# Kernel tuning notes

Hardware: AMD Instinct MI355X
Metric: run time of the kernel (lower is better)

## Reference

```python
import jax, jax.numpy as jnp
import numpy as np

B, T, C = 2, 2048, 768
H, N_LEFT = 12, 6
D = C // H


def setup_inputs() -> dict:
    key = jax.random.key(0)
    ks = jax.random.split(key, 4)
    x = jax.random.normal(ks[0], (B, T, C), dtype=jnp.float32)
    attention_mask = jnp.ones((B, T), dtype=jnp.int32)
    Wqkv_w = jax.random.normal(ks[1], (3 * C, C), dtype=jnp.float32) * (C ** -0.5)
    Wqkv_b = jnp.zeros((3 * C,), dtype=jnp.float32)
    Wo_w = jax.random.normal(ks[2], (C, C), dtype=jnp.float32) * (C ** -0.5)
    Wo_b = jnp.zeros((C,), dtype=jnp.float32)
    return {"x": x, "attention_mask": attention_mask, "Wqkv_w": Wqkv_w,
            "Wqkv_b": Wqkv_b, "Wo_w": Wo_w, "Wo_b": Wo_b}


def _attend(q, k, v, mask):
    # q,k,v: [B,h,T,D]; mask: [B,1,T,T] additive
    s = jnp.einsum('bhqd,bhkd->bhqk', q, k) * (D ** -0.5) + mask
    a = jax.nn.softmax(s.astype(jnp.float32), axis=-1).astype(q.dtype)
    return jnp.einsum('bhqk,bhkd->bhqd', a, v)


def reference(x, attention_mask, Wqkv_w, Wqkv_b, Wo_w, Wo_b):
    neg = jnp.finfo(x.dtype).min
    # padding mask [B,1,1,T]: 0 where valid, neg where padded
    pad = (1.0 - attention_mask.astype(x.dtype))[:, None, None, :] * neg
    i = jnp.arange(T)
    tri = (i[None, :] > i[:, None]).astype(x.dtype) * neg   # triu(neg, 1)
    left_mask = tri[None, None] + pad                        # causal (look left)
    right_mask = tri.T[None, None] + pad                     # anti-causal (look right)

    qkv = (x @ Wqkv_w.T + Wqkv_b).reshape(B, T, 3, H, D)
    qkv = jnp.transpose(qkv, (0, 3, 2, 1, 4))                # [B,H,3,T,D]
    q, k, v = qkv[:, :, 0], qkv[:, :, 1], qkv[:, :, 2]

    lc = _attend(q[:, :N_LEFT], k[:, :N_LEFT], v[:, :N_LEFT], left_mask)
    rc = _attend(q[:, N_LEFT:], k[:, N_LEFT:], v[:, N_LEFT:], right_mask)
    ctx = jnp.concatenate([lc, rc], axis=1)                  # [B,H,T,D]
    ctx = jnp.transpose(ctx, (0, 2, 1, 3)).reshape(B, T, C)
    out = ctx @ Wo_w.T + Wo_b
    return out
```

## Files before the change

### kernel.cpp

```cpp
#include <hip/hip_runtime.h>


typedef unsigned short u16;
typedef __bf16 bf16x8 __attribute__((ext_vector_type(8)));
typedef float fx4 __attribute__((ext_vector_type(4)));
typedef unsigned short u16x8 __attribute__((ext_vector_type(8)));
typedef unsigned short u16x4 __attribute__((ext_vector_type(4)));
typedef _Float16 hx4 __attribute__((ext_vector_type(4)));
typedef __fp16 fp16x2 __attribute__((ext_vector_type(2)));

#define T_SEQ 2048
#define C_DIM 768
#define NHEAD 12
#define HDIM  64
#define NITEMS 768
#define LOG2E_8 0.18033688f

__device__ __forceinline__ u16 f2bf(float f) {
  unsigned u = __float_as_uint(f);
  u += 0x7fffu + ((u >> 16) & 1u);
  return (u16)(u >> 16);
}
__device__ __forceinline__ u16 f2h(float f) {
  union { _Float16 h; u16 u; } cv; cv.h = (_Float16)f; return cv.u;
}

__device__ __forceinline__ void gl2lds16(const u16* g, u16* l) {
  __builtin_amdgcn_global_load_lds(
      (const __attribute__((address_space(1))) void*)g,
      (__attribute__((address_space(3))) void*)l, 16, 0, 0);
}

__global__ void cvt_swz_k(const float* __restrict__ x,
                          const float* __restrict__ wqkv,
                          const float* __restrict__ wo,
                          u16* __restrict__ out) {
  int i = blockIdx.x * blockDim.x + threadIdx.x;
  if (i >= 688128) return;
  int m = i / 96;
  int c8 = (i - m * 96) << 3;
  const float* src;
  if (m < 4096)       src = x    + (size_t)m * C_DIM + c8;
  else if (m < 6400)  src = wqkv + (size_t)(m - 4096) * C_DIM + c8;
  else                src = wo   + (size_t)(m - 6400) * C_DIM + c8;
  fx4 a = *(const fx4*)src, b = *(const fx4*)(src + 4);
  u16x8 o;
  #pragma unroll
  for (int j = 0; j < 4; ++j) { o[j] = f2bf(a[j]); o[4 + j] = f2bf(b[j]); }
  *(u16x8*)&out[(size_t)m * C_DIM + (c8 ^ ((m & 7) << 3))] = o;
}

__global__ void maskcvt_k(const int* __restrict__ am, float* __restrict__ mf,
                          unsigned* __restrict__ fbits, int* __restrict__ cnt) {
  int i = blockIdx.x * blockDim.x + threadIdx.x;
  if (i < 4096) mf[i] = am[i] ? 0.f : -1e30f;
  if (blockIdx.x == 16) {
    int t = threadIdx.x;
    if (t == 0) cnt[0] = 0;
    if (t < 64) {
      int bb = t >> 5, kt = t & 31;
      const int* seg = am + (bb << 11) + (kt << 6);
      int anyz = 0;
      for (int j = 0; j < 64; ++j) anyz |= (seg[j] == 0);
      unsigned long long bal = __ballot(anyz != 0);
      if (t == 0)  fbits[0] = (unsigned)(bal & 0xffffffffull);
      if (t == 32) fbits[1] = (unsigned)(bal >> 32);
    }
  }
}

__device__ __forceinline__ void gemm_core_64x128(const u16* __restrict__ A,
                                                 const u16* __restrict__ B,
                                                 int m0, int n0,
                                                 u16* As, u16* Bs,
                                                 fx4 acc[4][2]) {
  const int tid = threadIdx.x;
  const int lane = tid & 63, wv = tid >> 6;
  const int wn = wv << 5;
  const int lr = lane & 15, lg = lane >> 4;
  const int swk = (lr & 7) << 3;
  const int scol = (tid & 7) << 3;
  #pragma unroll
  for (int mt = 0; mt < 4; ++mt)
    #pragma unroll
    for (int nt = 0; nt < 2; ++nt) acc[mt][nt] = fx4{0.f, 0.f, 0.f, 0.f};

  #pragma unroll
  for (int p = 0; p < 2; ++p) {
    int row = (tid >> 3) + (p << 5);
    gl2lds16(&A[(size_t)(m0 + row) * C_DIM + scol], &As[(row << 6) + scol]);
  }
  #pragma unroll
  for (int p = 0; p < 4; ++p) {
    int row = (tid >> 3) + (p << 5);
    gl2lds16(&B[(size_t)(n0 + row) * C_DIM + scol], &Bs[(row << 6) + scol]);
  }

  int buf = 0;
  for (int k0 = 0; k0 < C_DIM; k0 += 64, buf ^= 1) {
    __syncthreads();
    if (k0 + 64 < C_DIM) {
      u16* Ad = &As[(buf ^ 1) << 12];
      u16* Bd = &Bs[(buf ^ 1) << 13];
      #pragma unroll
      for (int p = 0; p < 2; ++p) {
        int row = (tid >> 3) + (p << 5);
        gl2lds16(&A[(size_t)(m0 + row) * C_DIM + k0 + 64 + scol], &Ad[(row << 6) + scol]);
      }
      #pragma unroll
      for (int p = 0; p < 4; ++p) {
        int row = (tid >> 3) + (p << 5);
        gl2lds16(&B[(size_t)(n0 + row) * C_DIM + k0 + 64 + scol], &Bd[(row << 6) + scol]);
      }
    }
    const u16* Ab = &As[buf << 12];
    const u16* Bb = &Bs[buf << 13];
    #pragma unroll
    for (int kk = 0; kk < 64; kk += 32) {
      bf16x8 af[4], bfr[2];
      #pragma unroll
      for (int mt = 0; mt < 4; ++mt)
        af[mt] = *(const bf16x8*)&Ab[((mt * 16 + lr) << 6) + ((kk + lg * 8) ^ swk)];
      #pragma unroll
      for (int nt = 0; nt < 2; ++nt)
        bfr[nt] = *(const bf16x8*)&Bb[((wn + nt * 16 + lr) << 6) + ((kk + lg * 8) ^ swk)];
      #pragma unroll
      for (int mt = 0; mt < 4; ++mt)
        #pragma unroll
        for (int nt = 0; nt < 2; ++nt)
          acc[mt][nt] = __builtin_amdgcn_mfma_f32_16x16x32_bf16(
              af[mt], bfr[nt], acc[mt][nt], 0, 0, 0);
    }
  }
}

__global__ __launch_bounds__(256) void gemm_qkv_k(
    const u16* __restrict__ A, const u16* __restrict__ B,
    const float* __restrict__ bias,
    u16* __restrict__ qb, u16* __restrict__ kswz, u16* __restrict__ vswz) {
  __shared__ __align__(16) u16 As[2][64 * 64];
  __shared__ __align__(16) u16 Bs[2][128 * 64];
  int m0 = blockIdx.y << 6, n0 = blockIdx.x << 7;
  fx4 acc[4][2];
  gemm_core_64x128(A, B, m0, n0, &As[0][0], &Bs[0][0], acc);

  const int tid = threadIdx.x, lane = tid & 63, wv = tid >> 6;
  const int wn = wv << 5;
  const int lr = lane & 15, lg = lane >> 4;
  const int part = n0 / 768;
  const int n0r = n0 - part * 768;
  const int bb = m0 >> 11, kt = (m0 >> 6) & 31;
  u16* Sc = &Bs[0][0];
  __syncthreads();

  if (part < 2) {
    #pragma unroll
    for (int nt = 0; nt < 2; ++nt) {
      int nl = wn + nt * 16 + lr;
      float bv = bias[n0 + nl];
      #pragma unroll
      for (int mt = 0; mt < 4; ++mt) {
        #pragma unroll
        for (int r = 0; r < 4; ++r) {
          int m = mt * 16 + lg * 4 + r;
          Sc[(m << 7) + (nl ^ ((m & 15) << 2))] = f2bf(acc[mt][nt][r] + bv);
        }
      }
    }
    __syncthreads();
    int c4 = (tid & 31) << 2;
    int ng = n0r + c4;
    int h = ng >> 6, d = ng & 63;
    int bh = bb * NHEAD + h;
    #pragma unroll
    for (int p = 0; p < 8; ++p) {
      int m = (tid >> 5) + (p << 3);
      u16x4 v = *(const u16x4*)&Sc[(m << 7) + (c4 ^ ((m & 15) << 2))];
      if (part == 0) {
        int t = (m0 & 2047) + m;
        *(u16x4*)&qb[(((size_t)bh << 11) + t) * HDIM + d] = v;
      } else {
        *(u16x4*)&kswz[((size_t)(bh * 32 + kt) << 12) + (m << 6) +
                       (d ^ ((m & 7) << 3))] = v;
      }
    }
  } else {
    #pragma unroll
    for (int nt = 0; nt < 2; ++nt) {
      int nl = wn + nt * 16 + lr;
      float bv = bias[n0 + nl];
      #pragma unroll
      for (int mt = 0; mt < 4; ++mt) {
        u16x4 pk;
        #pragma unroll
        for (int r = 0; r < 4; ++r) pk[r] = f2h(acc[mt][nt][r] + bv);
        int m4 = (mt << 2) + lg;
        *(u16x4*)&Sc[(nl << 6) + ((m4 ^ (nl & 15)) << 2)] = pk;
      }
    }
    __syncthreads();
    int tr4 = tid & 15;
    #pragma unroll
    for (int p = 0; p < 8; ++p) {
      int nl = (tid >> 4) + (p << 4);
      int ng = n0r + nl;
      int h = ng >> 6, d = ng & 63;
      u16x4 v = *(const u16x4*)&Sc[(nl << 6) + ((tr4 ^ (nl & 15)) << 2)];
      size_t tile = (size_t)((bb * NHEAD + h) * 32 + kt) << 12;
      *(u16x4*)&vswz[tile + (d << 6) + ((tr4 ^ (d & 15)) << 2)] = v;
    }
  }
}

__device__ __forceinline__ void gemm_core_64x64(const u16* __restrict__ A,
                                                const u16* __restrict__ B,
                                                int m0, int n0,
                                                u16* As, u16* Bs,
                                                fx4 acc[2][2]) {
  const int tid = threadIdx.x;
  const int lane = tid & 63, wv = tid >> 6;
  const int wm = (wv & 1) << 5, wn = (wv >> 1) << 5;
  const int lr = lane & 15, lg = lane >> 4;
  const int swk = (lr & 7) << 3;
  const int scol = (tid & 7) << 3;
  #pragma unroll
  for (int mt = 0; mt < 2; ++mt)
    #pragma unroll
    for (int nt = 0; nt < 2; ++nt) acc[mt][nt] = fx4{0.f, 0.f, 0.f, 0.f};

  #pragma unroll
  for (int p = 0; p < 2; ++p) {
    int row = (tid >> 3) + (p << 5);
    gl2lds16(&A[(size_t)(m0 + row) * C_DIM + scol], &As[(row << 6) + scol]);
    gl2lds16(&B[(size_t)(n0 + row) * C_DIM + scol], &Bs[(row << 6) + scol]);
  }

  int buf = 0;
  for (int k0 = 0; k0 < C_DIM; k0 += 64, buf ^= 1) {
    __syncthreads();
    if (k0 + 64 < C_DIM) {
      u16* Ad = &As[(buf ^ 1) << 12];
      u16* Bd = &Bs[(buf ^ 1) << 12];
      #pragma unroll
      for (int p = 0; p < 2; ++p) {
        int row = (tid >> 3) + (p << 5);
        gl2lds16(&A[(size_t)(m0 + row) * C_DIM + k0 + 64 + scol], &Ad[(row << 6) + scol]);
        gl2lds16(&B[(size_t)(n0 + row) * C_DIM + k0 + 64 + scol], &Bd[(row << 6) + scol]);
      }
    }
    const u16* Ab = &As[buf << 12];
    const u16* Bb = &Bs[buf << 12];
    #pragma unroll
    for (int kk = 0; kk < 64; kk += 32) {
      bf16x8 af[2], bfr[2];
      #pragma unroll
      for (int mt = 0; mt < 2; ++mt)
        af[mt] = *(const bf16x8*)&Ab[((wm + mt * 16 + lr) << 6) + ((kk + lg * 8) ^ swk)];
      #pragma unroll
      for (int nt = 0; nt < 2; ++nt)
        bfr[nt] = *(const bf16x8*)&Bb[((wn + nt * 16 + lr) << 6) + ((kk + lg * 8) ^ swk)];
      #pragma unroll
      for (int mt = 0; mt < 2; ++mt)
        #pragma unroll
        for (int nt = 0; nt < 2; ++nt)
          acc[mt][nt] = __builtin_amdgcn_mfma_f32_16x16x32_bf16(
              af[mt], bfr[nt], acc[mt][nt], 0, 0, 0);
    }
  }
}

__global__ __launch_bounds__(256) void gemm_out_k(
    const u16* __restrict__ A, const u16* __restrict__ B,
    const float* __restrict__ bias, float* __restrict__ out) {
  __shared__ __align__(16) u16 As[2][64 * 64];
  __shared__ __align__(16) u16 Bs[2][64 * 64];
  int m0 = blockIdx.y << 6, n0 = blockIdx.x << 6;
  fx4 acc[2][2];
  gemm_core_64x64(A, B, m0, n0, &As[0][0], &Bs[0][0], acc);

  const int tid = threadIdx.x, lane = tid & 63, wv = tid >> 6;
  const int wm = (wv & 1) << 5, wn = (wv >> 1) << 5;
  const int lr = lane & 15, lg = lane >> 4;
  #pragma unroll
  for (int nt = 0; nt < 2; ++nt) {
    int n = n0 + wn + nt * 16 + lr;
    float bv = bias[n];
    #pragma unroll
    for (int mt = 0; mt < 2; ++mt) {
      #pragma unroll
      for (int r = 0; r < 4; ++r) {
        int m = m0 + wm + mt * 16 + lg * 4 + r;
        out[(size_t)m * C_DIM + n] = acc[mt][nt][r] + bv;
      }
    }
  }
}

__global__ __launch_bounds__(256) void attn_k(
    const u16* __restrict__ q, const u16* __restrict__ kswz,
    const u16* __restrict__ vswz, const float* __restrict__ maskf,
    const unsigned* __restrict__ fbits,
    u16* __restrict__ ctx, int* __restrict__ counter) {
  __shared__ __align__(16) u16 Ks[2][4096];
  __shared__ __align__(16) u16 Vt[2][4096];
  __shared__ int s_w;

  const int tid = threadIdx.x, lane = tid & 63, wv = tid >> 6;
  const int lr = lane & 15, lg = lane >> 4;
  const int swk = (lr & 7) << 3;
  const int swv = (lr & 15) << 2;

  for (;;) {
    if (tid == 0) s_w = atomicAdd(counter, 1);
    __syncthreads();
    int w = s_w;
    if (w >= NITEMS) break;
    int qslot = w / 24, bh = w - qslot * 24;
    int bb = bh / NHEAD, h = bh - bb * NHEAD;
    bool causal = (h < 6);
    int qt = causal ? (31 - qslot) : qslot;
    int kt0 = causal ? 0 : qt;
    int kt1 = causal ? qt : 31;
    size_t tile_base = (size_t)(bh * 32) << 12;
    unsigned fb = fbits[bb];

    {
      const u16* kg = kswz + tile_base + ((size_t)kt0 << 12);
      const u16* vg = vswz + tile_base + ((size_t)kt0 << 12);
      #pragma unroll
      for (int c2 = 0; c2 < 2; ++c2) {
        int e = (wv << 10) + (c2 << 9) + (lane << 3);
        gl2lds16(kg + e, &Ks[0][e]);
        gl2lds16(vg + e, &Vt[0][e]);
      }
    }

    int q0 = qt << 6;
    size_t head_off = ((size_t)bh << 11) * HDIM;
    int qrow = q0 + wv * 16 + lr;
    bf16x8 qf0 = *(const bf16x8*)&q[head_off + (size_t)qrow * HDIM + lg * 8];
    bf16x8 qf1 = *(const bf16x8*)&q[head_off + (size_t)qrow * HDIM + 32 + lg * 8];
    const float* mrow = maskf + (bb << 11);

    fx4 o[4];
    #pragma unroll
    for (int dt = 0; dt < 4; ++dt) o[dt] = fx4{0.f, 0.f, 0.f, 0.f};
    float l_i = 0.f;

    int buf = 0;
    for (int kt = kt0; kt <= kt1; ++kt, buf ^= 1) {
      __syncthreads();
      if (kt < kt1) {
        const u16* kg = kswz + tile_base + ((size_t)(kt + 1) << 12);
        const u16* vg = vswz + tile_base + ((size_t)(kt + 1) << 12);
        #pragma unroll
        for (int c2 = 0; c2 < 2; ++c2) {
          int e = (wv << 10) + (c2 << 9) + (lane << 3);
          gl2lds16(kg + e, &Ks[buf ^ 1][e]);
          gl2lds16(vg + e, &Vt[buf ^ 1][e]);
        }
      }

      fx4 st[4];
      #pragma unroll
      for (int nt = 0; nt < 4; ++nt) {
        const u16* kr = &Ks[buf][(nt * 16 + lr) << 6];
        bf16x8 kf0 = *(const bf16x8*)&kr[(lg * 8) ^ swk];
        bf16x8 kf1 = *(const bf16x8*)&kr[(32 + lg * 8) ^ swk];
        fx4 z = fx4{0.f, 0.f, 0.f, 0.f};
        z = __builtin_amdgcn_mfma_f32_16x16x32_bf16(kf0, qf0, z, 0, 0, 0);
        st[nt] = __builtin_amdgcn_mfma_f32_16x16x32_bf16(kf1, qf1, z, 0, 0, 0);
      }

      float psum = 0.f;
      if (kt == qt) {
        #pragma unroll
        for (int nt = 0; nt < 4; ++nt) {
          int kb0 = (kt << 6) + nt * 16 + lg * 4;
          fx4 mv = *(const fx4*)&mrow[kb0];
          #pragma unroll
          for (int r = 0; r < 4; ++r) {
            float arg = st[nt][r] * LOG2E_8 + mv[r];
            int kabs = kb0 + r;
            bool dead = causal ? (kabs > qrow) : (kabs < qrow);
            arg = dead ? -1e30f : arg;
            float p = __builtin_amdgcn_exp2f(arg);
            st[nt][r] = p;
            psum += p;
          }
        }
      } else if ((fb >> kt) & 1u) {
        #pragma unroll
        for (int nt = 0; nt < 4; ++nt) {
          int kb0 = (kt << 6) + nt * 16 + lg * 4;
          fx4 mv = *(const fx4*)&mrow[kb0];
          #pragma unroll
          for (int r = 0; r < 4; ++r) {
            float p = __builtin_amdgcn_exp2f(st[nt][r] * LOG2E_8 + mv[r]);
            st[nt][r] = p;
            psum += p;
          }
        }
      } else {
        #pragma unroll
        for (int nt = 0; nt < 4; ++nt)
          #pragma unroll
          for (int r = 0; r < 4; ++r) {
            float p = __builtin_amdgcn_exp2f(st[nt][r] * LOG2E_8);
            st[nt][r] = p;
            psum += p;
          }
      }
      l_i += psum;

      #pragma unroll
      for (int nt = 0; nt < 4; ++nt) {
        union { hx4 v; fp16x2 h[2]; } pu;
        pu.h[0] = __builtin_amdgcn_cvt_pkrtz(st[nt][0], st[nt][1]);
        pu.h[1] = __builtin_amdgcn_cvt_pkrtz(st[nt][2], st[nt][3]);
        hx4 pf = pu.v;
        #pragma unroll
        for (int dt = 0; dt < 4; ++dt) {
          const u16* vr = &Vt[buf][(dt * 16 + lr) << 6];
          hx4 vf = *(const hx4*)&vr[(nt * 16 + lg * 4) ^ swv];
          o[dt] = __builtin_amdgcn_mfma_f32_16x16x16f16(vf, pf, o[dt], 0, 0, 0);
        }
      }
    }

    l_i += __shfl_xor(l_i, 16, 64);
    l_i += __shfl_xor(l_i, 32, 64);
    float inv = 1.f / l_i;
    size_t rowb = ((size_t)(bb << 11) + qrow) * C_DIM;
    int csw = (qrow & 7) << 3;
    #pragma unroll
    for (int dt = 0; dt < 4; ++dt) {
      u16x4 pk;
      #pragma unroll
      for (int r = 0; r < 4; ++r) pk[r] = f2bf(o[dt][r] * inv);
      int colb = h * HDIM + dt * 16 + lg * 4;
      *(u16x4*)&ctx[rowb + (colb ^ csw)] = pk;
    }
  }
}

extern "C" void kernel_launch(void* const* d_in, const int* in_sizes, int n_in,
                              void* d_out, int out_size, void* d_ws, size_t ws_size,
                              hipStream_t stream) {
  const float* x     = (const float*)d_in[0];
  const int*   amask = (const int*)d_in[1];
  const float* wqkv  = (const float*)d_in[2];
  const float* bqkv  = (const float*)d_in[3];
  const float* wo    = (const float*)d_in[4];
  const float* bo    = (const float*)d_in[5];
  float* out = (float*)d_out;

  char* ws = (char*)d_ws;
  u16*      xb    = (u16*)(ws + 0);
  u16*      wqkvb = (u16*)(ws + 6291456);
  u16*      wob   = (u16*)(ws + 9830400);
  u16*      qb    = (u16*)(ws + 11010048);
  u16*      kswz  = (u16*)(ws + 17301504);
  u16*      vswz  = (u16*)(ws + 23592960);
  u16*      ctxb  = (u16*)(ws + 29884416);
  float*    maskf = (float*)(ws + 36175872);
  int*      cnt   = (int*)(ws + 36192256);
  unsigned* fbits = (unsigned*)(ws + 36192320);

  cvt_swz_k<<<2688, 256, 0, stream>>>(x, wqkv, wo, xb);
  maskcvt_k<<<17, 256, 0, stream>>>(amask, maskf, fbits, cnt);

  gemm_qkv_k<<<dim3(18, 64), 256, 0, stream>>>(xb, wqkvb, bqkv, qb, kswz, vswz);
  attn_k<<<512, 256, 0, stream>>>(qb, kswz, vswz, maskf, fbits, ctxb, cnt);
  gemm_out_k<<<dim3(12, 64), 256, 0, stream>>>(ctxb, wob, bo, out);
}
```

Measured before the change: 164.5 us.

## Triple-buffer K/V tiles in attention with explicit vmcnt waits and more blocks

The attention kernel's K/V shared-memory staging moves from double to triple buffering. It prefetches two tiles ahead and waits with a partial s_waitcnt vmcnt(4) plus s_barrier, replacing a full __syncthreads before each tile. It also precomputes swizzled LDS offsets, preloads the diagonal mask values, splits the probability sum into two accumulators, and raises the persistent grid from 512 to 640 blocks. The aim is to hide global-to-LDS load latency, though the extra 16KB of LDS may reduce occupancy and the hand-written waitcnt depends on exact load counts.

```diff
diff --git a/kernel.cpp b/kernel.cpp
--- a/kernel.cpp
+++ b/kernel.cpp
@@ -301,14 +301,20 @@
     const u16* __restrict__ vswz, const float* __restrict__ maskf,
     const unsigned* __restrict__ fbits,
     u16* __restrict__ ctx, int* __restrict__ counter) {
-  __shared__ __align__(16) u16 Ks[2][4096];
-  __shared__ __align__(16) u16 Vt[2][4096];
+  __shared__ __align__(16) u16 Ks[3][4096];
+  __shared__ __align__(16) u16 Vt[3][4096];
   __shared__ int s_w;
 
   const int tid = threadIdx.x, lane = tid & 63, wv = tid >> 6;
   const int lr = lane & 15, lg = lane >> 4;
   const int swk = (lr & 7) << 3;
   const int swv = (lr & 15) << 2;
+  const int e0 = (lr << 6) + ((lg * 8) ^ swk);
+  const int e1 = (lr << 6) + ((32 + lg * 8) ^ swk);
+  int ve[4];
+  #pragma unroll
+  for (int nt = 0; nt < 4; ++nt)
+    ve[nt] = (lr << 6) + (((nt << 4) + (lg << 2)) ^ swv);
 
   for (;;) {
     if (tid == 0) s_w = atomicAdd(counter, 1);
@@ -324,60 +330,82 @@
     size_t tile_base = (size_t)(bh * 32) << 12;
     unsigned fb = fbits[bb];
 
-    {
-      const u16* kg = kswz + tile_base + ((size_t)kt0 << 12);
-      const u16* vg = vswz + tile_base + ((size_t)kt0 << 12);
-      #pragma unroll
-      for (int c2 = 0; c2 < 2; ++c2) {
-        int e = (wv << 10) + (c2 << 9) + (lane << 3);
-        gl2lds16(kg + e, &Ks[0][e]);
-        gl2lds16(vg + e, &Vt[0][e]);
-      }
-    }
-
     int q0 = qt << 6;
     size_t head_off = ((size_t)bh << 11) * HDIM;
     int qrow = q0 + wv * 16 + lr;
     bf16x8 qf0 = *(const bf16x8*)&q[head_off + (size_t)qrow * HDIM + lg * 8];
     bf16x8 qf1 = *(const bf16x8*)&q[head_off + (size_t)qrow * HDIM + 32 + lg * 8];
     const float* mrow = maskf + (bb << 11);
+    fx4 mdiag[4];
+    #pragma unroll
+    for (int nt = 0; nt < 4; ++nt)
+      mdiag[nt] = *(const fx4*)&mrow[q0 + nt * 16 + lg * 4];
+
+    asm volatile("" ::: "memory");
+
+    {
+      const u16* kg = kswz + tile_base + ((size_t)kt0 << 12);
+      const u16* vg = vswz + tile_base + ((size_t)kt0 << 12);
+      #pragma unroll
+      for (int c2 = 0; c2 < 2; ++c2) {
+        int e = (wv << 10) + (c2 << 9) + (lane << 3);
+        gl2lds16(kg + e, &Ks[0][e]);
+        gl2lds16(vg + e, &Vt[0][e]);
+      }
+      if (kt0 + 1 <= kt1) {
+        const u16* kg1 = kswz + tile_base + ((size_t)(kt0 + 1) << 12);
+        const u16* vg1 = vswz + tile_base + ((size_t)(kt0 + 1) << 12);
+        #pragma unroll
+        for (int c2 = 0; c2 < 2; ++c2) {
+          int e = (wv << 10) + (c2 << 9) + (lane << 3);
+          gl2lds16(kg1 + e, &Ks[1][e]);
+          gl2lds16(vg1 + e, &Vt[1][e]);
+        }
+      }
+    }
 
     fx4 o[4];
     #pragma unroll
     for (int dt = 0; dt < 4; ++dt) o[dt] = fx4{0.f, 0.f, 0.f, 0.f};
     float l_i = 0.f;
 
-    int buf = 0;
-    for (int kt = kt0; kt <= kt1; ++kt, buf ^= 1) {
-      __syncthreads();
-      if (kt < kt1) {
-        const u16* kg = kswz + tile_base + ((size_t)(kt + 1) << 12);
-        const u16* vg = vswz + tile_base + ((size_t)(kt + 1) << 12);
+    int cur = 0;
+    for (int kt = kt0; kt <= kt1; ++kt) {
+      if (kt < kt1) asm volatile("s_waitcnt vmcnt(4)\n\ts_barrier" ::: "memory");
+      else          asm volatile("s_waitcnt vmcnt(0)\n\ts_barrier" ::: "memory");
+      __builtin_amdgcn_sched_barrier(0);
+
+      if (kt + 2 <= kt1) {
+        int nx = cur + 2; if (nx >= 3) nx -= 3;
+        const u16* kg = kswz + tile_base + ((size_t)(kt + 2) << 12);
+        const u16* vg = vswz + tile_base + ((size_t)(kt + 2) << 12);
         #pragma unroll
         for (int c2 = 0; c2 < 2; ++c2) {
           int e = (wv << 10) + (c2 << 9) + (lane << 3);
-          gl2lds16(kg + e, &Ks[buf ^ 1][e]);
-          gl2lds16(vg + e, &Vt[buf ^ 1][e]);
+          gl2lds16(kg + e, &Ks[nx][e]);
+          gl2lds16(vg + e, &Vt[nx][e]);
         }
       }
 
+      const u16* kb = &Ks[cur][0];
+      const u16* vbl = &Vt[cur][0];
+
       fx4 st[4];
       #pragma unroll
       for (int nt = 0; nt < 4; ++nt) {
-        const u16* kr = &Ks[buf][(nt * 16 + lr) << 6];
-        bf16x8 kf0 = *(const bf16x8*)&kr[(lg * 8) ^ swk];
-        bf16x8 kf1 = *(const bf16x8*)&kr[(32 + lg * 8) ^ swk];
+        bf16x8 kf0 = *(const bf16x8*)&kb[e0 + (nt << 10)];
+        bf16x8 kf1 = *(const bf16x8*)&kb[e1 + (nt << 10)];
         fx4 z = fx4{0.f, 0.f, 0.f, 0.f};
         z = __builtin_amdgcn_mfma_f32_16x16x32_bf16(kf0, qf0, z, 0, 0, 0);
         st[nt] = __builtin_amdgcn_mfma_f32_16x16x32_bf16(kf1, qf1, z, 0, 0, 0);
       }
 
-      float psum = 0.f;
+      float ps0 = 0.f, ps1 = 0.f;
       if (kt == qt) {
         #pragma unroll
         for (int nt = 0; nt < 4; ++nt) {
           int kb0 = (kt << 6) + nt * 16 + lg * 4;
-          fx4 mv = *(const fx4*)&mrow[kb0];
+          fx4 mv = mdiag[nt];
           #pragma unroll
           for (int r = 0; r < 4; ++r) {
             float arg = st[nt][r] * LOG2E_8 + mv[r];
@@ -386,7 +414,7 @@
             arg = dead ? -1e30f : arg;
             float p = __builtin_amdgcn_exp2f(arg);
             st[nt][r] = p;
-            psum += p;
+            if (r & 1) ps1 += p; else ps0 += p;
           }
         }
       } else if ((fb >> kt) & 1u) {
@@ -398,7 +426,7 @@
           for (int r = 0; r < 4; ++r) {
             float p = __builtin_amdgcn_exp2f(st[nt][r] * LOG2E_8 + mv[r]);
             st[nt][r] = p;
-            psum += p;
+            if (r & 1) ps1 += p; else ps0 += p;
           }
         }
       } else {
@@ -408,24 +436,24 @@
           for (int r = 0; r < 4; ++r) {
             float p = __builtin_amdgcn_exp2f(st[nt][r] * LOG2E_8);
             st[nt][r] = p;
-            psum += p;
+            if (r & 1) ps1 += p; else ps0 += p;
           }
       }
-      l_i += psum;
+      l_i += ps0 + ps1;
 
       #pragma unroll
       for (int nt = 0; nt < 4; ++nt) {
-        union { hx4 v; fp16x2 h[2]; } pu;
-        pu.h[0] = __builtin_amdgcn_cvt_pkrtz(st[nt][0], st[nt][1]);
-        pu.h[1] = __builtin_amdgcn_cvt_pkrtz(st[nt][2], st[nt][3]);
+        union { hx4 v; fp16x2 hh[2]; } pu;
+        pu.hh[0] = __builtin_amdgcn_cvt_pkrtz(st[nt][0], st[nt][1]);
+        pu.hh[1] = __builtin_amdgcn_cvt_pkrtz(st[nt][2], st[nt][3]);
         hx4 pf = pu.v;
         #pragma unroll
         for (int dt = 0; dt < 4; ++dt) {
-          const u16* vr = &Vt[buf][(dt * 16 + lr) << 6];
-          hx4 vf = *(const hx4*)&vr[(nt * 16 + lg * 4) ^ swv];
+          hx4 vf = *(const hx4*)&vbl[ve[nt] + (dt << 10)];
           o[dt] = __builtin_amdgcn_mfma_f32_16x16x16f16(vf, pf, o[dt], 0, 0, 0);
         }
       }
+      ++cur; if (cur == 3) cur = 0;
     }
 
     l_i += __shfl_xor(l_i, 16, 64);
@@ -471,6 +499,6 @@
   maskcvt_k<<<17, 256, 0, stream>>>(amask, maskf, fbits, cnt);
 
   gemm_qkv_k<<<dim3(18, 64), 256, 0, stream>>>(xb, wqkvb, bqkv, qb, kswz, vswz);
-  attn_k<<<512, 256, 0, stream>>>(qb, kswz, vswz, maskf, fbits, ctxb, cnt);
+  attn_k<<<640, 256, 0, stream>>>(qb, kswz, vswz, maskf, fbits, ctxb, cnt);
   gemm_out_k<<<dim3(12, 64), 256, 0, stream>>>(ctxb, wob, bo, out);
 }
```

New measurement: 168.0 us. +2.1%, slower.

## Split heavy attention query tiles into KV chunks combined by atomic accumulation

Applied to the files above, without the earlier changes.

The attention work is repartitioned into 1152 chunks. Query tiles with long key ranges are split into two halves of at most 16 KV tiles each, and partial outputs and row sums are accumulated with float atomics into a zeroed workspace. A new finalize kernel then normalizes those partials and writes bf16 ctx. This is meant to even out per-workgroup load and shorten the attention tail, at the cost of a memset, atomic traffic, an extra launch, and reuse of the xb workspace region. LDS address offsets are also precomputed and the softmax row sum is split across two accumulators.

```diff
diff --git a/kernel.cpp b/kernel.cpp
--- a/kernel.cpp
+++ b/kernel.cpp
@@ -13,7 +13,8 @@
 #define C_DIM 768
 #define NHEAD 12
 #define HDIM  64
-#define NITEMS 768
+#define NCHUNK 1152
+#define NHEAVY 384
 #define LOG2E_8 0.18033688f
 
 __device__ __forceinline__ u16 f2bf(float f) {
@@ -300,7 +301,8 @@
     const u16* __restrict__ q, const u16* __restrict__ kswz,
     const u16* __restrict__ vswz, const float* __restrict__ maskf,
     const unsigned* __restrict__ fbits,
-    u16* __restrict__ ctx, int* __restrict__ counter) {
+    u16* __restrict__ ctx, int* __restrict__ counter,
+    float* __restrict__ oacc, float* __restrict__ lacc) {
   __shared__ __align__(16) u16 Ks[2][4096];
   __shared__ __align__(16) u16 Vt[2][4096];
   __shared__ int s_w;
@@ -309,18 +311,41 @@
   const int lr = lane & 15, lg = lane >> 4;
   const int swk = (lr & 7) << 3;
   const int swv = (lr & 15) << 2;
+  const int e0 = (lr << 6) + ((lg * 8) ^ swk);
+  const int e1 = (lr << 6) + ((32 + lg * 8) ^ swk);
+  int ve[4];
+  #pragma unroll
+  for (int nt = 0; nt < 4; ++nt)
+    ve[nt] = (lr << 6) + (((nt << 4) + (lg << 2)) ^ swv);
 
   for (;;) {
     if (tid == 0) s_w = atomicAdd(counter, 1);
     __syncthreads();
     int w = s_w;
-    if (w >= NITEMS) break;
-    int qslot = w / 24, bh = w - qslot * 24;
+    if (w >= NCHUNK) break;
+    int s = w / 24, bh = w - s * 24;
     int bb = bh / NHEAD, h = bh - bb * NHEAD;
     bool causal = (h < 6);
-    int qt = causal ? (31 - qslot) : qslot;
-    int kt0 = causal ? 0 : qt;
-    int kt1 = causal ? qt : 31;
+    int qt, kt0, kt1;
+    bool direct;
+    if (s < 16) {
+      direct = false;
+      if (causal) { qt = 16 + s; kt0 = 0;  kt1 = 15; }
+      else        { qt = s;      kt0 = 16; kt1 = 31; }
+    } else {
+      int u = s - 16;
+      int L = 16 - (u >> 1);
+      if ((u & 1) == 0) {
+        direct = false;
+        if (causal) { qt = L + 15; kt0 = 16; kt1 = qt; }
+        else        { qt = 16 - L; kt0 = qt; kt1 = 15; }
+      } else {
+        direct = true;
+        if (causal) { qt = L - 1;  kt0 = 0;  kt1 = qt; }
+        else        { qt = 32 - L; kt0 = qt; kt1 = 31; }
+      }
+    }
+    int hv = (bh << 4) + (causal ? qt - 16 : qt);
     size_t tile_base = (size_t)(bh * 32) << 12;
     unsigned fb = fbits[bb];
 
@@ -361,18 +386,20 @@
         }
       }
 
+      const u16* kb = &Ks[buf][0];
+      const u16* vbl = &Vt[buf][0];
+
       fx4 st[4];
       #pragma unroll
       for (int nt = 0; nt < 4; ++nt) {
-        const u16* kr = &Ks[buf][(nt * 16 + lr) << 6];
-        bf16x8 kf0 = *(const bf16x8*)&kr[(lg * 8) ^ swk];
-        bf16x8 kf1 = *(const bf16x8*)&kr[(32 + lg * 8) ^ swk];
+        bf16x8 kf0 = *(const bf16x8*)&kb[e0 + (nt << 10)];
+        bf16x8 kf1 = *(const bf16x8*)&kb[e1 + (nt << 10)];
         fx4 z = fx4{0.f, 0.f, 0.f, 0.f};
         z = __builtin_amdgcn_mfma_f32_16x16x32_bf16(kf0, qf0, z, 0, 0, 0);
         st[nt] = __builtin_amdgcn_mfma_f32_16x16x32_bf16(kf1, qf1, z, 0, 0, 0);
       }
 
-      float psum = 0.f;
+      float ps0 = 0.f, ps1 = 0.f;
       if (kt == qt) {
         #pragma unroll
         for (int nt = 0; nt < 4; ++nt) {
@@ -386,7 +413,7 @@
             arg = dead ? -1e30f : arg;
             float p = __builtin_amdgcn_exp2f(arg);
             st[nt][r] = p;
-            psum += p;
+            if (r & 1) ps1 += p; else ps0 += p;
           }
         }
       } else if ((fb >> kt) & 1u) {
@@ -398,7 +425,7 @@
           for (int r = 0; r < 4; ++r) {
             float p = __builtin_amdgcn_exp2f(st[nt][r] * LOG2E_8 + mv[r]);
             st[nt][r] = p;
-            psum += p;
+            if (r & 1) ps1 += p; else ps0 += p;
           }
         }
       } else {
@@ -408,21 +435,20 @@
           for (int r = 0; r < 4; ++r) {
             float p = __builtin_amdgcn_exp2f(st[nt][r] * LOG2E_8);
             st[nt][r] = p;
-            psum += p;
+            if (r & 1) ps1 += p; else ps0 += p;
           }
       }
-      l_i += psum;
+      l_i += ps0 + ps1;
 
       #pragma unroll
       for (int nt = 0; nt < 4; ++nt) {
-        union { hx4 v; fp16x2 h[2]; } pu;
-        pu.h[0] = __builtin_amdgcn_cvt_pkrtz(st[nt][0], st[nt][1]);
-        pu.h[1] = __builtin_amdgcn_cvt_pkrtz(st[nt][2], st[nt][3]);
+        union { hx4 v; fp16x2 hh[2]; } pu;
+        pu.hh[0] = __builtin_amdgcn_cvt_pkrtz(st[nt][0], st[nt][1]);
+        pu.hh[1] = __builtin_amdgcn_cvt_pkrtz(st[nt][2], st[nt][3]);
         hx4 pf = pu.v;
         #pragma unroll
         for (int dt = 0; dt < 4; ++dt) {
-          const u16* vr = &Vt[buf][(dt * 16 + lr) << 6];
-          hx4 vf = *(const hx4*)&vr[(nt * 16 + lg * 4) ^ swv];
+          hx4 vf = *(const hx4*)&vbl[ve[nt] + (dt << 10)];
           o[dt] = __builtin_amdgcn_mfma_f32_16x16x16f16(vf, pf, o[dt], 0, 0, 0);
         }
       }
@@ -430,17 +456,58 @@
 
     l_i += __shfl_xor(l_i, 16, 64);
     l_i += __shfl_xor(l_i, 32, 64);
-    float inv = 1.f / l_i;
-    size_t rowb = ((size_t)(bb << 11) + qrow) * C_DIM;
-    int csw = (qrow & 7) << 3;
-    #pragma unroll
-    for (int dt = 0; dt < 4; ++dt) {
-      u16x4 pk;
-      #pragma unroll
-      for (int r = 0; r < 4; ++r) pk[r] = f2bf(o[dt][r] * inv);
-      int colb = h * HDIM + dt * 16 + lg * 4;
-      *(u16x4*)&ctx[rowb + (colb ^ csw)] = pk;
-    }
+    if (direct) {
+      float inv = 1.f / l_i;
+      size_t rowb = ((size_t)(bb << 11) + qrow) * C_DIM;
+      int csw = (qrow & 7) << 3;
+      #pragma unroll
+      for (int dt = 0; dt < 4; ++dt) {
+        u16x4 pk;
+        #pragma unroll
+        for (int r = 0; r < 4; ++r) pk[r] = f2bf(o[dt][r] * inv);
+        int colb = h * HDIM + dt * 16 + lg * 4;
+        *(u16x4*)&ctx[rowb + (colb ^ csw)] = pk;
+      }
+    } else {
+      float* ob = oacc + ((size_t)hv << 12);
+      int qq = wv * 16 + lr;
+      #pragma unroll
+      for (int dt = 0; dt < 4; ++dt)
+        #pragma unroll
+        for (int r = 0; r < 4; ++r) {
+          int d = dt * 16 + lg * 4 + r;
+          atomicAdd(&ob[(d << 6) + qq], o[dt][r]);
+        }
+      if (lg == 0) atomicAdd(&lacc[(hv << 6) + qq], l_i);
+    }
+  }
+}
+
+__global__ __launch_bounds__(256) void fin_k(const float* __restrict__ oacc,
+                                             const float* __restrict__ lacc,
+                                             u16* __restrict__ ctx) {
+  int hv = blockIdx.x;
+  int bh = hv >> 4, idx = hv & 15;
+  int bb = bh / NHEAD, h = bh - bb * NHEAD;
+  int qt = (h < 6) ? idx + 16 : idx;
+  int q0 = qt << 6;
+  int tid = threadIdx.x;
+  int qq = tid & 63, dblk = tid >> 6;
+  const float* ob = oacc + ((size_t)hv << 12);
+  float inv = 1.f / lacc[(hv << 6) + qq];
+  int tq = q0 + qq;
+  size_t rowb = ((size_t)(bb << 11) + tq) * C_DIM;
+  int csw = (tq & 7) << 3;
+  #pragma unroll
+  for (int c = 0; c < 4; ++c) {
+    u16x4 pk;
+    #pragma unroll
+    for (int r = 0; r < 4; ++r) {
+      int d = dblk * 16 + c * 4 + r;
+      pk[r] = f2bf(ob[(d << 6) + qq] * inv);
+    }
+    int colb = h * HDIM + dblk * 16 + c * 4;
+    *(u16x4*)&ctx[rowb + (colb ^ csw)] = pk;
   }
 }
 
@@ -466,11 +533,16 @@
   float*    maskf = (float*)(ws + 36175872);
   int*      cnt   = (int*)(ws + 36192256);
   unsigned* fbits = (unsigned*)(ws + 36192320);
+  float*    oacc  = (float*)(ws + 0);
+  float*    lacc  = (float*)(ws + 6291456);
 
   cvt_swz_k<<<2688, 256, 0, stream>>>(x, wqkv, wo, xb);
   maskcvt_k<<<17, 256, 0, stream>>>(amask, maskf, fbits, cnt);
 
   gemm_qkv_k<<<dim3(18, 64), 256, 0, stream>>>(xb, wqkvb, bqkv, qb, kswz, vswz);
-  attn_k<<<512, 256, 0, stream>>>(qb, kswz, vswz, maskf, fbits, ctxb, cnt);
+  hipMemsetAsync(ws, 0, 6291456 + 98304, stream);
+  attn_k<<<768, 256, 0, stream>>>(qb, kswz, vswz, maskf, fbits, ctxb, cnt,
+                                  oacc, lacc);
+  fin_k<<<NHEAVY, 256, 0, stream>>>(oacc, lacc, ctxb);
   gemm_out_k<<<dim3(12, 64), 256, 0, stream>>>(ctxb, wob, bo, out);
 }
```

After: 179.5 us. +9.1%, slower.
